# Optimization experiments

Measured on AMD Instinct MI355X. Metric: run time of the kernel, lower is better.

## Reference

```python
import jax, jax.numpy as jnp
import numpy as np

B, T, D, H = 2, 2048, 1024, 16
DH = D // H  # head dim = 64


def setup_inputs() -> dict:
    key = jax.random.key(0)
    ks = jax.random.split(key, 10)
    s = D ** -0.5
    inp = {
        "x": jax.random.normal(ks[0], (B, T, D), jnp.float32),
        "data_mask": jax.random.randint(ks[1], (B, T), 0, 2, jnp.int32),
        "Wq": jax.random.normal(ks[2], (D, D), jnp.float32) * s,
        "bq": jnp.zeros((D,), jnp.float32),
        "Wk": jax.random.normal(ks[3], (D, D), jnp.float32) * s,
        "bk": jnp.zeros((D,), jnp.float32),
        "Wv": jax.random.normal(ks[4], (D, D), jnp.float32) * s,
        "bv": jnp.zeros((D,), jnp.float32),
        "Wp": jax.random.normal(ks[5], (D, D), jnp.float32) * s,
        "bp": jnp.zeros((D,), jnp.float32),
    }
    return inp


def _split_heads(t):
    # [B, T, D] -> [B, H, T, DH]
    return jnp.swapaxes(t.reshape(B, T, H, DH), 1, 2)


def reference(x, data_mask, Wq, bq, Wk, bk, Wv, bv, Wp, bp):
    q = _split_heads(x @ Wq + bq)
    k = _split_heads(x @ Wk + bk)  # kv = x (self-attention)
    v = _split_heads(x @ Wv + bv)

    # combined mask: causal tri AND data_mask outer product -> [B, 1, T, T]
    dm = data_mask.astype(bool)
    causal = jnp.tril(jnp.ones((T, T), bool))
    mask = causal[None, None] & (dm[:, None, :, None] & dm[:, None, None, :])

    q = q * (DH ** -0.5)  # scale_logits
    scores = jnp.einsum('bhqd,bhkd->bhqk', q, k)  # [B, H, T, T]
    scores = jnp.where(mask, scores, -jnp.inf)
    weights = jax.nn.softmax(scores, axis=-1)
    weights = jnp.nan_to_num(weights)  # fully-masked rows -> 0
    o = jnp.einsum('bhqk,bhkd->bhqd', weights, v)

    # recover shape: [B, H, T, DH] -> [B, T, D]
    o = jnp.swapaxes(o, 1, 2).reshape(B, T, D)
    o = o @ Wp + bp

    # linear mask: multiply output by data_mask [B, T, 1]
    o = o * data_mask.astype(o.dtype)[..., None]
    return o
```

## Files before the change

### kernel.cpp

```cpp
#include <hip/hip_runtime.h>
#include <hip/hip_bf16.h>
#include <cstdint>
#include <cstddef>

#define Bb 2
#define Tt 2048
#define Dd 1024
#define Hh 16
#define DHh 64

using short8 = __attribute__((ext_vector_type(8))) short;
using f32x4  = __attribute__((ext_vector_type(4))) float;
typedef unsigned short u16;

__device__ __forceinline__ u16 f2bf(float f) {
    unsigned int u = __float_as_uint(f);
    u += 0x7fffu + ((u >> 16) & 1u);
    return (u16)(u >> 16);
}

__device__ __forceinline__ unsigned int pk2bf(float a, float b) {
    union { __hip_bfloat162 h; unsigned int u; } c;
    c.h = __float22bfloat162_rn(float2{a, b});
    return c.u;
}

__device__ __forceinline__ void gload16(const void* g, void* l) {
    __builtin_amdgcn_global_load_lds((const __attribute__((address_space(1))) void*)g,
                                     (__attribute__((address_space(3))) void*)l, 16, 0, 0);
}

__device__ __forceinline__ void gemm_bt_core(const u16* __restrict__ A, const u16* __restrict__ BT,
                                             int K, int m0, int n0,
                                             u16* As, u16* Bs, f32x4 acc[4][4]) {
    const int tid = threadIdx.x;
    const int w = tid >> 6, lane = tid & 63;
    const int lr = lane & 15, lg = lane >> 4;
    const int wr = w >> 1, wc = w & 1;
    const int arow = lane >> 2;
    const int acol = (lane & 3) * 8;
    for (int kk = 0; kk < K; kk += 32) {
        __syncthreads();
#pragma unroll
        for (int j = 0; j < 2; ++j) {
            int r0 = w * 32 + j * 16;
            gload16(A  + (size_t)(m0 + r0 + arow) * K + kk + acol, (char*)As + r0 * 64);
            gload16(BT + (size_t)(n0 + r0 + arow) * K + kk + acol, (char*)Bs + r0 * 64);
        }
        __syncthreads();
        short8 af[4], bfv[4];
#pragma unroll
        for (int m = 0; m < 4; ++m)
            af[m] = *(const short8*)((const char*)As + ((wr * 64 + m * 16 + lr) * 64 + lg * 16));
#pragma unroll
        for (int n = 0; n < 4; ++n)
            bfv[n] = *(const short8*)((const char*)Bs + ((wc * 64 + n * 16 + lr) * 64 + lg * 16));
#pragma unroll
        for (int m = 0; m < 4; ++m)
#pragma unroll
            for (int n = 0; n < 4; ++n)
                acc[m][n] = __builtin_amdgcn_mfma_f32_16x16x32_bf16(af[m], bfv[n], acc[m][n], 0, 0, 0);
    }
}

__global__ __launch_bounds__(256) void convert_x_k(const float4* __restrict__ x4,
                                                   ushort4* __restrict__ xb4, int n4) {
    int i = blockIdx.x * 256 + threadIdx.x;
    if (i >= n4) return;
    float4 v = x4[i];
    ushort4 o;
    o.x = f2bf(v.x); o.y = f2bf(v.y); o.z = f2bf(v.z); o.w = f2bf(v.w);
    xb4[i] = o;
}

__global__ void transpose_w_k(const float* __restrict__ Wq, const float* __restrict__ Wk,
                              const float* __restrict__ Wv, const float* __restrict__ Wp,
                              u16* __restrict__ wt) {
    __shared__ float tile[32][33];
    const int z = blockIdx.z;
    const float* W = (z == 0) ? Wq : (z == 1) ? Wk : (z == 2) ? Wv : Wp;
    const int n0 = blockIdx.x * 32, k0 = blockIdx.y * 32;
    const int tx = threadIdx.x, ty = threadIdx.y;
#pragma unroll
    for (int j = 0; j < 4; ++j)
        tile[ty + j * 8][tx] = W[(size_t)(k0 + ty + j * 8) * Dd + n0 + tx];
    __syncthreads();
    u16* outp = wt + (size_t)z * Dd * Dd;
#pragma unroll
    for (int j = 0; j < 4; ++j)
        outp[(size_t)(n0 + ty + j * 8) * Dd + k0 + tx] = f2bf(tile[tx][ty + j * 8]);
}

__global__ __launch_bounds__(256) void qkv_gemm_k(const u16* __restrict__ xb, const u16* __restrict__ wt,
        const float* __restrict__ bq, const float* __restrict__ bk, const float* __restrict__ bv,
        u16* __restrict__ Qg, u16* __restrict__ Kg, u16* __restrict__ VTg) {
    __shared__ alignas(16) u16 As[128 * 32];
    __shared__ alignas(16) u16 Bs[128 * 32];
    f32x4 acc[4][4];
    const f32x4 vzero = {0.f, 0.f, 0.f, 0.f};
#pragma unroll
    for (int m = 0; m < 4; ++m)
#pragma unroll
        for (int n = 0; n < 4; ++n) acc[m][n] = vzero;
    const int m0 = blockIdx.y * 128, n0 = blockIdx.x * 128;
    gemm_bt_core(xb, wt, 1024, m0, n0, As, Bs, acc);
    const int tid = threadIdx.x, w = tid >> 6, lane = tid & 63, lr = lane & 15, lg = lane >> 4;
    const int wr = w >> 1, wc = w & 1;
    const int sec = n0 >> 10;
    const float* bias = (sec == 0) ? bq : (sec == 1) ? bk : bv;
    u16* dst = (sec == 0) ? Qg : (sec == 1) ? Kg : VTg;
    const float qscale = (sec == 0) ? 0.125f * 1.4426950408889634f : 1.0f;
#pragma unroll
    for (int n = 0; n < 4; ++n) {
        int gn = n0 + wc * 64 + n * 16 + lr;
        int j = gn & 1023;
        float bj = bias[j];
        int h = j >> 6, dh = j & 63;
#pragma unroll
        for (int m = 0; m < 4; ++m) {
            int gmb = m0 + wr * 64 + m * 16 + 4 * lg;
#pragma unroll
            for (int i = 0; i < 4; ++i) {
                int gm = gmb + i;
                int b = gm >> 11, t = gm & 2047;
                float v = (acc[m][n][i] + bj) * qscale;
                size_t off;
                if (sec < 2) off = (((size_t)(b * Hh + h)) * Tt + t) * DHh + dh;
                else         off = (((size_t)(b * Hh + h)) * DHh + dh) * Tt + t;
                dst[off] = f2bf(v);
            }
        }
    }
}

__global__ __launch_bounds__(256) void attn_k(const u16* __restrict__ Qg, const u16* __restrict__ Kg,
        const u16* __restrict__ VTg, const int* __restrict__ dmask, u16* __restrict__ Og) {
    __shared__ alignas(16) u16 Ks[128 * 64];
    __shared__ alignas(16) u16 Vs[64 * 128];
    __shared__ alignas(16) u16 Ps[4][16 * 128];
    const int bh = blockIdx.x;
    const int qb = (int)gridDim.y - 1 - (int)blockIdx.y;
    const int b = bh >> 4, h = bh & 15;
    const int tid = threadIdx.x, w = tid >> 6, lane = tid & 63;
    const int lr = lane & 15, lg = lane >> 4;
    const int q0 = qb * 64 + w * 16;
    const int qrow = q0 + lr;
    const u16* Qbase = Qg + ((size_t)bh * Tt + q0) * DHh;
    short8 qf0 = *(const short8*)(Qbase + lr * DHh + lg * 8);
    short8 qf1 = *(const short8*)(Qbase + lr * DHh + 32 + lg * 8);
    const f32x4 vzero = {0.f, 0.f, 0.f, 0.f};
    float mrow = -1e30f, lrow = 0.f;
    f32x4 o[4];
#pragma unroll
    for (int n = 0; n < 4; ++n) o[n] = vzero;
    const int ktiles = (qb * 64 + 63) / 128 + 1;
    char* KsB = (char*)Ks; char* VsB = (char*)Vs; char* PsB = (char*)&Ps[w][0];

    for (int kt = 0; kt < ktiles; ++kt) {
        const int kbase = kt * 128;
        __syncthreads();
#pragma unroll
        for (int j = 0; j < 4; ++j) {
            int r0 = w * 32 + j * 8;
            int r = r0 + (lane >> 3);
            int cs = (lane & 7) ^ (r & 7);
            gload16(Kg + ((size_t)bh * Tt + kbase + r) * DHh + cs * 8, KsB + r0 * 128);
        }
#pragma unroll
        for (int j = 0; j < 4; ++j) {
            int r0 = w * 16 + j * 4;
            int r = r0 + (lane >> 4);
            int cs = (lane & 15) ^ (r & 7);
            gload16(VTg + ((size_t)bh * DHh + r) * Tt + kbase + cs * 8, VsB + r0 * 256);
        }
        __syncthreads();
        f32x4 s[8];
#pragma unroll
        for (int nf = 0; nf < 8; ++nf) {
            int r = nf * 16 + lr;
            short8 k0v = *(const short8*)(KsB + r * 128 + (((0 + lg) ^ (r & 7)) << 4));
            short8 k1v = *(const short8*)(KsB + r * 128 + (((4 + lg) ^ (r & 7)) << 4));
            f32x4 t0 = __builtin_amdgcn_mfma_f32_16x16x32_bf16(k0v, qf0, vzero, 0, 0, 0);
            s[nf] = __builtin_amdgcn_mfma_f32_16x16x32_bf16(k1v, qf1, t0, 0, 0, 0);
        }
        float4 km[8];
        {
            const int4* dmv = (const int4*)(dmask + (size_t)b * Tt + kbase);
#pragma unroll
            for (int nf = 0; nf < 8; ++nf) {
                int4 mi = dmv[4 * nf + lg];
                km[nf] = make_float4((float)mi.x, (float)mi.y, (float)mi.z, (float)mi.w);
            }
        }
        if (kbase + 127 > q0) {
#pragma unroll
            for (int nf = 0; nf < 8; ++nf) {
                int tk = kbase + 16 * nf + 4 * lg;
                if (tk + 0 > qrow) km[nf].x = 0.f;
                if (tk + 1 > qrow) km[nf].y = 0.f;
                if (tk + 2 > qrow) km[nf].z = 0.f;
                if (tk + 3 > qrow) km[nf].w = 0.f;
            }
        }
        float rm;
        {
            f32x4 m4 = s[0];
#pragma unroll
            for (int nf = 1; nf < 8; ++nf) {
                m4[0] = fmaxf(m4[0], s[nf][0]); m4[1] = fmaxf(m4[1], s[nf][1]);
                m4[2] = fmaxf(m4[2], s[nf][2]); m4[3] = fmaxf(m4[3], s[nf][3]);
            }
            rm = fmaxf(fmaxf(m4[0], m4[1]), fmaxf(m4[2], m4[3]));
            rm = fmaxf(rm, __shfl_xor(rm, 16));
            rm = fmaxf(rm, __shfl_xor(rm, 32));
        }
        float mn = fmaxf(mrow, rm);
        float sc = exp2f(mrow - mn);
        mrow = mn;
        lrow *= sc;
#pragma unroll
        for (int n = 0; n < 4; ++n) {
            o[n][0] *= sc; o[n][1] *= sc; o[n][2] *= sc; o[n][3] *= sc;
        }
        float rs = 0.f;
#pragma unroll
        for (int nf = 0; nf < 8; ++nf) {
            float p0 = exp2f(s[nf][0] - mn) * km[nf].x;
            float p1 = exp2f(s[nf][1] - mn) * km[nf].y;
            float p2 = exp2f(s[nf][2] - mn) * km[nf].z;
            float p3 = exp2f(s[nf][3] - mn) * km[nf].w;
            rs += (p0 + p1) + (p2 + p3);
            uint2 pw;
            pw.x = pk2bf(p0, p1);
            pw.y = pk2bf(p2, p3);
            *(uint2*)(PsB + lr * 256 + ((((2 * nf + (lg >> 1)) ^ (lr & 7))) << 4) + ((lg & 1) << 3)) = pw;
        }
        rs += __shfl_xor(rs, 16);
        rs += __shfl_xor(rs, 32);
        lrow += rs;
#pragma unroll
        for (int ks = 0; ks < 4; ++ks) {
            short8 pf = *(const short8*)(PsB + lr * 256 + ((((ks * 4 + lg)) ^ (lr & 7)) << 4));
#pragma unroll
            for (int n = 0; n < 4; ++n) {
                int rv = n * 16 + lr;
                short8 vf = *(const short8*)(VsB + rv * 256 + ((((ks * 4 + lg)) ^ (rv & 7)) << 4));
                o[n] = __builtin_amdgcn_mfma_f32_16x16x32_bf16(vf, pf, o[n], 0, 0, 0);
            }
        }
    }
    float inv = lrow > 0.f ? 1.0f / lrow : 0.f;
#pragma unroll
    for (int n = 0; n < 4; ++n) {
        uint2 pw;
        pw.x = pk2bf(o[n][0] * inv, o[n][1] * inv);
        pw.y = pk2bf(o[n][2] * inv, o[n][3] * inv);
        *(uint2*)(Og + ((size_t)(b * Tt + qrow)) * Dd + h * DHh + n * 16 + 4 * lg) = pw;
    }
}

__global__ __launch_bounds__(256) void out_gemm_k(const u16* __restrict__ Og, const u16* __restrict__ wpt,
        const float* __restrict__ bp, const int* __restrict__ dmask, float* __restrict__ out) {
    __shared__ alignas(16) u16 As[128 * 32];
    __shared__ alignas(16) u16 Bs[128 * 32];
    f32x4 acc[4][4];
    const f32x4 vzero = {0.f, 0.f, 0.f, 0.f};
#pragma unroll
    for (int m = 0; m < 4; ++m)
#pragma unroll
        for (int n = 0; n < 4; ++n) acc[m][n] = vzero;
    const int m0 = blockIdx.y * 128, n0 = blockIdx.x * 128;
    gemm_bt_core(Og, wpt, 1024, m0, n0, As, Bs, acc);
    const int tid = threadIdx.x, w = tid >> 6, lane = tid & 63, lr = lane & 15, lg = lane >> 4;
    const int wr = w >> 1, wc = w & 1;
#pragma unroll
    for (int n = 0; n < 4; ++n) {
        int gn = n0 + wc * 64 + n * 16 + lr;
        float bj = bp[gn];
#pragma unroll
        for (int m = 0; m < 4; ++m) {
            int gmb = m0 + wr * 64 + m * 16 + 4 * lg;
#pragma unroll
            for (int i = 0; i < 4; ++i) {
                int gm = gmb + i;
                float dmv = (float)dmask[gm];
                out[(size_t)gm * Dd + gn] = (acc[m][n][i] + bj) * dmv;
            }
        }
    }
}

extern "C" void kernel_launch(void* const* d_in, const int* in_sizes, int n_in,
                              void* d_out, int out_size, void* d_ws, size_t ws_size,
                              hipStream_t stream) {
    const float* x   = (const float*)d_in[0];
    const int*  dmask = (const int*)d_in[1];
    const float* Wq = (const float*)d_in[2];
    const float* bq = (const float*)d_in[3];
    const float* Wk = (const float*)d_in[4];
    const float* bk = (const float*)d_in[5];
    const float* Wv = (const float*)d_in[6];
    const float* bv = (const float*)d_in[7];
    const float* Wp = (const float*)d_in[8];
    const float* bp = (const float*)d_in[9];
    float* out = (float*)d_out;
    char* ws = (char*)d_ws;
    u16* xb  = (u16*)(ws);
    u16* wt  = (u16*)(ws + ((size_t)8 << 20));
    u16* Qg  = (u16*)(ws + ((size_t)16 << 20));
    u16* Kg  = (u16*)(ws + ((size_t)24 << 20));
    u16* VTg = (u16*)(ws + ((size_t)32 << 20));
    u16* Og  = xb;

    convert_x_k<<<dim3(4096), dim3(256), 0, stream>>>((const float4*)x, (ushort4*)xb, (Bb * Tt * Dd) / 4);
    transpose_w_k<<<dim3(32, 32, 4), dim3(32, 8), 0, stream>>>(Wq, Wk, Wv, Wp, wt);
    qkv_gemm_k<<<dim3(24, 32), dim3(256), 0, stream>>>(xb, wt, bq, bk, bv, Qg, Kg, VTg);
    attn_k<<<dim3(32, 32), dim3(256), 0, stream>>>(Qg, Kg, VTg, dmask, Og);
    out_gemm_k<<<dim3(8, 32), dim3(256), 0, stream>>>(Og, wt + (size_t)3 * Dd * Dd, bp, dmask, out);
}
```

Measured before the change: 132.3 us.

## Restructure attention with 32x32 MFMA, 128-row query blocks and double-buffered K/V tiles

Rewrites the attention kernel so each block handles 128 query rows (32 per wave) using 32x32x16 bf16 MFMAs. K/V tiles shrink to 64 keys and are double-buffered, so the next tile's async load overlaps compute. P is passed between lanes with cross-lane shuffles instead of an LDS round trip. The grid halves to 512 blocks, which lowers parallelism and makes per-block work more unbalanced across the causal range, and register pressure rises with the 16-wide accumulators.

```diff
diff --git a/kernel.cpp b/kernel.cpp
--- a/kernel.cpp
+++ b/kernel.cpp
@@ -11,6 +11,7 @@
 
 using short8 = __attribute__((ext_vector_type(8))) short;
 using f32x4  = __attribute__((ext_vector_type(4))) float;
+using f32x16 = __attribute__((ext_vector_type(16))) float;
 typedef unsigned short u16;
 
 __device__ __forceinline__ u16 f2bf(float f) {
@@ -133,129 +134,149 @@
     }
 }
 
-__global__ __launch_bounds__(256) void attn_k(const u16* __restrict__ Qg, const u16* __restrict__ Kg,
+__global__ __launch_bounds__(256, 2) void attn_k(const u16* __restrict__ Qg, const u16* __restrict__ Kg,
         const u16* __restrict__ VTg, const int* __restrict__ dmask, u16* __restrict__ Og) {
-    __shared__ alignas(16) u16 Ks[128 * 64];
-    __shared__ alignas(16) u16 Vs[64 * 128];
-    __shared__ alignas(16) u16 Ps[4][16 * 128];
+    __shared__ alignas(16) u16 Ks[2][64 * 64];
+    __shared__ alignas(16) u16 Vs[2][64 * 64];
     const int bh = blockIdx.x;
-    const int qb = (int)gridDim.y - 1 - (int)blockIdx.y;
+    const int qb = 15 - (int)blockIdx.y;
     const int b = bh >> 4, h = bh & 15;
     const int tid = threadIdx.x, w = tid >> 6, lane = tid & 63;
-    const int lr = lane & 15, lg = lane >> 4;
-    const int q0 = qb * 64 + w * 16;
-    const int qrow = q0 + lr;
-    const u16* Qbase = Qg + ((size_t)bh * Tt + q0) * DHh;
-    short8 qf0 = *(const short8*)(Qbase + lr * DHh + lg * 8);
-    short8 qf1 = *(const short8*)(Qbase + lr * DHh + 32 + lg * 8);
-    const f32x4 vzero = {0.f, 0.f, 0.f, 0.f};
+    const int lq = lane & 31, hi = lane >> 5;
+    const int q0w = qb * 128 + w * 32;
+    const int qrow = q0w + lq;
+    short8 qf[4];
+    {
+        const u16* Qbase = Qg + ((size_t)bh * Tt + qrow) * DHh;
+#pragma unroll
+        for (int ks = 0; ks < 4; ++ks) qf[ks] = *(const short8*)(Qbase + ks * 16 + hi * 8);
+    }
+    f32x16 ot0, ot1;
+#pragma unroll
+    for (int i = 0; i < 16; ++i) { ot0[i] = 0.f; ot1[i] = 0.f; }
     float mrow = -1e30f, lrow = 0.f;
-    f32x4 o[4];
-#pragma unroll
-    for (int n = 0; n < 4; ++n) o[n] = vzero;
-    const int ktiles = (qb * 64 + 63) / 128 + 1;
-    char* KsB = (char*)Ks; char* VsB = (char*)Vs; char* PsB = (char*)&Ps[w][0];
-
-    for (int kt = 0; kt < ktiles; ++kt) {
-        const int kbase = kt * 128;
+    const int rr = lane >> 3, cc = lane & 7;
+
+#define STAGE(BUF, KB) do { \
+    _Pragma("unroll") \
+    for (int j = 0; j < 2; ++j) { \
+        int r0 = w * 16 + j * 8; \
+        gload16(Kg  + ((size_t)bh * Tt  + (KB) + r0 + rr) * DHh + ((cc ^ rr) * 8), (char*)&Ks[BUF][0] + r0 * 128); \
+        gload16(VTg + ((size_t)bh * DHh + r0 + rr) * Tt + (KB) + ((cc ^ rr) * 8), (char*)&Vs[BUF][0] + r0 * 128); \
+    } } while (0)
+
+    const int nkt = 2 * qb + 2;
+    int buf = 0;
+    STAGE(0, 0);
+    __syncthreads();
+    for (int kt = 0; kt < nkt; ++kt) {
+        const int kb = kt * 64;
+        if (kt + 1 < nkt) {
+            if (buf) STAGE(0, kb + 64); else STAGE(1, kb + 64);
+        }
+        if (kb <= q0w + 31) {
+            const char* KsB = (const char*)&Ks[buf][0];
+            const char* VsB = (const char*)&Vs[buf][0];
+            const int swz = lq & 7;
+            f32x16 st0, st1;
+#pragma unroll
+            for (int i = 0; i < 16; ++i) { st0[i] = 0.f; st1[i] = 0.f; }
+#pragma unroll
+            for (int ks = 0; ks < 4; ++ks) {
+                short8 kf0 = *(const short8*)(KsB + lq * 128        + (((2 * ks + hi) ^ swz) << 4));
+                short8 kf1 = *(const short8*)(KsB + (32 + lq) * 128 + (((2 * ks + hi) ^ swz) << 4));
+                st0 = __builtin_amdgcn_mfma_f32_32x32x16_bf16(kf0, qf[ks], st0, 0, 0, 0);
+                st1 = __builtin_amdgcn_mfma_f32_32x32x16_bf16(kf1, qf[ks], st1, 0, 0, 0);
+            }
+            float4 km[8];
+            {
+                const int4* dmv = (const int4*)(dmask + (size_t)b * Tt + kb);
+#pragma unroll
+                for (int t = 0; t < 2; ++t)
+#pragma unroll
+                    for (int g = 0; g < 4; ++g) {
+                        int4 mi = dmv[t * 8 + g * 2 + hi];
+                        km[t * 4 + g] = make_float4((float)mi.x, (float)mi.y, (float)mi.z, (float)mi.w);
+                    }
+            }
+            if (kb + 63 > q0w) {
+#pragma unroll
+                for (int t = 0; t < 2; ++t)
+#pragma unroll
+                    for (int g = 0; g < 4; ++g) {
+                        int k4 = kb + 32 * t + 8 * g + 4 * hi;
+                        float4& m4 = km[t * 4 + g];
+                        if (k4 + 0 > qrow) m4.x = 0.f;
+                        if (k4 + 1 > qrow) m4.y = 0.f;
+                        if (k4 + 2 > qrow) m4.z = 0.f;
+                        if (k4 + 3 > qrow) m4.w = 0.f;
+                    }
+            }
+            float rm = st0[0];
+#pragma unroll
+            for (int i = 1; i < 16; ++i) rm = fmaxf(rm, st0[i]);
+#pragma unroll
+            for (int i = 0; i < 16; ++i) rm = fmaxf(rm, st1[i]);
+            rm = fmaxf(rm, __shfl_xor(rm, 32));
+            float mn = fmaxf(mrow, rm);
+            float sc = exp2f(mrow - mn);
+            mrow = mn;
+            lrow *= sc;
+#pragma unroll
+            for (int i = 0; i < 16; ++i) { ot0[i] *= sc; ot1[i] *= sc; }
+            float rs = 0.f;
+#pragma unroll
+            for (int s = 0; s < 4; ++s) {
+                float p[8];
+#pragma unroll
+                for (int e = 0; e < 8; ++e) {
+                    float sv = (s < 2) ? ((s & 1) ? st0[8 + e] : st0[e])
+                                       : ((s & 1) ? st1[8 + e] : st1[e]);
+                    float mv;
+                    {
+                        const float4& m4 = km[(s >> 1) * 4 + (s & 1) * 2 + (e >> 2)];
+                        int e3 = e & 3;
+                        mv = (e3 == 0) ? m4.x : (e3 == 1) ? m4.y : (e3 == 2) ? m4.z : m4.w;
+                    }
+                    p[e] = exp2f(sv - mn) * mv;
+                    rs += p[e];
+                }
+                unsigned a0 = pk2bf(p[0], p[1]), a1 = pk2bf(p[2], p[3]);
+                unsigned b0 = pk2bf(p[4], p[5]), b1 = pk2bf(p[6], p[7]);
+                unsigned sa0 = __shfl_xor(a0, 32), sa1 = __shfl_xor(a1, 32);
+                unsigned sb0 = __shfl_xor(b0, 32), sb1 = __shfl_xor(b1, 32);
+                union { uint4 u; short8 sv; } pf;
+                pf.u.x = hi ? sb0 : a0;
+                pf.u.y = hi ? sb1 : a1;
+                pf.u.z = hi ? b0 : sa0;
+                pf.u.w = hi ? b1 : sa1;
+                short8 vf0 = *(const short8*)(VsB + lq * 128        + (((2 * s + hi) ^ swz) << 4));
+                short8 vf1 = *(const short8*)(VsB + (32 + lq) * 128 + (((2 * s + hi) ^ swz) << 4));
+                ot0 = __builtin_amdgcn_mfma_f32_32x32x16_bf16(vf0, pf.sv, ot0, 0, 0, 0);
+                ot1 = __builtin_amdgcn_mfma_f32_32x32x16_bf16(vf1, pf.sv, ot1, 0, 0, 0);
+            }
+            rs += __shfl_xor(rs, 32);
+            lrow += rs;
+        }
         __syncthreads();
-#pragma unroll
-        for (int j = 0; j < 4; ++j) {
-            int r0 = w * 32 + j * 8;
-            int r = r0 + (lane >> 3);
-            int cs = (lane & 7) ^ (r & 7);
-            gload16(Kg + ((size_t)bh * Tt + kbase + r) * DHh + cs * 8, KsB + r0 * 128);
-        }
-#pragma unroll
-        for (int j = 0; j < 4; ++j) {
-            int r0 = w * 16 + j * 4;
-            int r = r0 + (lane >> 4);
-            int cs = (lane & 15) ^ (r & 7);
-            gload16(VTg + ((size_t)bh * DHh + r) * Tt + kbase + cs * 8, VsB + r0 * 256);
-        }
-        __syncthreads();
-        f32x4 s[8];
-#pragma unroll
-        for (int nf = 0; nf < 8; ++nf) {
-            int r = nf * 16 + lr;
-            short8 k0v = *(const short8*)(KsB + r * 128 + (((0 + lg) ^ (r & 7)) << 4));
-            short8 k1v = *(const short8*)(KsB + r * 128 + (((4 + lg) ^ (r & 7)) << 4));
-            f32x4 t0 = __builtin_amdgcn_mfma_f32_16x16x32_bf16(k0v, qf0, vzero, 0, 0, 0);
-            s[nf] = __builtin_amdgcn_mfma_f32_16x16x32_bf16(k1v, qf1, t0, 0, 0, 0);
-        }
-        float4 km[8];
-        {
-            const int4* dmv = (const int4*)(dmask + (size_t)b * Tt + kbase);
-#pragma unroll
-            for (int nf = 0; nf < 8; ++nf) {
-                int4 mi = dmv[4 * nf + lg];
-                km[nf] = make_float4((float)mi.x, (float)mi.y, (float)mi.z, (float)mi.w);
-            }
-        }
-        if (kbase + 127 > q0) {
-#pragma unroll
-            for (int nf = 0; nf < 8; ++nf) {
-                int tk = kbase + 16 * nf + 4 * lg;
-                if (tk + 0 > qrow) km[nf].x = 0.f;
-                if (tk + 1 > qrow) km[nf].y = 0.f;
-                if (tk + 2 > qrow) km[nf].z = 0.f;
-                if (tk + 3 > qrow) km[nf].w = 0.f;
-            }
-        }
-        float rm;
-        {
-            f32x4 m4 = s[0];
-#pragma unroll
-            for (int nf = 1; nf < 8; ++nf) {
-                m4[0] = fmaxf(m4[0], s[nf][0]); m4[1] = fmaxf(m4[1], s[nf][1]);
-                m4[2] = fmaxf(m4[2], s[nf][2]); m4[3] = fmaxf(m4[3], s[nf][3]);
-            }
-            rm = fmaxf(fmaxf(m4[0], m4[1]), fmaxf(m4[2], m4[3]));
-            rm = fmaxf(rm, __shfl_xor(rm, 16));
-            rm = fmaxf(rm, __shfl_xor(rm, 32));
-        }
-        float mn = fmaxf(mrow, rm);
-        float sc = exp2f(mrow - mn);
-        mrow = mn;
-        lrow *= sc;
-#pragma unroll
-        for (int n = 0; n < 4; ++n) {
-            o[n][0] *= sc; o[n][1] *= sc; o[n][2] *= sc; o[n][3] *= sc;
-        }
-        float rs = 0.f;
-#pragma unroll
-        for (int nf = 0; nf < 8; ++nf) {
-            float p0 = exp2f(s[nf][0] - mn) * km[nf].x;
-            float p1 = exp2f(s[nf][1] - mn) * km[nf].y;
-            float p2 = exp2f(s[nf][2] - mn) * km[nf].z;
-            float p3 = exp2f(s[nf][3] - mn) * km[nf].w;
-            rs += (p0 + p1) + (p2 + p3);
+        buf ^= 1;
+    }
+#undef STAGE
+    float inv = lrow > 0.f ? 1.0f / lrow : 0.f;
+    u16* ob = Og + ((size_t)(b * Tt + qrow)) * Dd + h * DHh;
+#pragma unroll
+    for (int d = 0; d < 2; ++d) {
+#pragma unroll
+        for (int g = 0; g < 4; ++g) {
             uint2 pw;
-            pw.x = pk2bf(p0, p1);
-            pw.y = pk2bf(p2, p3);
-            *(uint2*)(PsB + lr * 256 + ((((2 * nf + (lg >> 1)) ^ (lr & 7))) << 4) + ((lg & 1) << 3)) = pw;
-        }
-        rs += __shfl_xor(rs, 16);
-        rs += __shfl_xor(rs, 32);
-        lrow += rs;
-#pragma unroll
-        for (int ks = 0; ks < 4; ++ks) {
-            short8 pf = *(const short8*)(PsB + lr * 256 + ((((ks * 4 + lg)) ^ (lr & 7)) << 4));
-#pragma unroll
-            for (int n = 0; n < 4; ++n) {
-                int rv = n * 16 + lr;
-                short8 vf = *(const short8*)(VsB + rv * 256 + ((((ks * 4 + lg)) ^ (rv & 7)) << 4));
-                o[n] = __builtin_amdgcn_mfma_f32_16x16x32_bf16(vf, pf, o[n], 0, 0, 0);
-            }
-        }
-    }
-    float inv = lrow > 0.f ? 1.0f / lrow : 0.f;
-#pragma unroll
-    for (int n = 0; n < 4; ++n) {
-        uint2 pw;
-        pw.x = pk2bf(o[n][0] * inv, o[n][1] * inv);
-        pw.y = pk2bf(o[n][2] * inv, o[n][3] * inv);
-        *(uint2*)(Og + ((size_t)(b * Tt + qrow)) * Dd + h * DHh + n * 16 + 4 * lg) = pw;
+            float v0 = (d ? ot1[4 * g + 0] : ot0[4 * g + 0]) * inv;
+            float v1 = (d ? ot1[4 * g + 1] : ot0[4 * g + 1]) * inv;
+            float v2 = (d ? ot1[4 * g + 2] : ot0[4 * g + 2]) * inv;
+            float v3 = (d ? ot1[4 * g + 3] : ot0[4 * g + 3]) * inv;
+            pw.x = pk2bf(v0, v1);
+            pw.y = pk2bf(v2, v3);
+            *(uint2*)(ob + d * 32 + g * 8 + hi * 4) = pw;
+        }
     }
 }
 
@@ -315,6 +336,6 @@
     convert_x_k<<<dim3(4096), dim3(256), 0, stream>>>((const float4*)x, (ushort4*)xb, (Bb * Tt * Dd) / 4);
     transpose_w_k<<<dim3(32, 32, 4), dim3(32, 8), 0, stream>>>(Wq, Wk, Wv, Wp, wt);
     qkv_gemm_k<<<dim3(24, 32), dim3(256), 0, stream>>>(xb, wt, bq, bk, bv, Qg, Kg, VTg);
-    attn_k<<<dim3(32, 32), dim3(256), 0, stream>>>(Qg, Kg, VTg, dmask, Og);
+    attn_k<<<dim3(32, 16), dim3(256), 0, stream>>>(Qg, Kg, VTg, dmask, Og);
     out_gemm_k<<<dim3(8, 32), dim3(256), 0, stream>>>(Og, wt + (size_t)3 * Dd * Dd, bp, dmask, out);
 }
```

Result: slower. 147.8 us (+11.7%).

## Replace QKV GEMM with 256x256-tile, 8-wave double-buffered pipelined kernel

Applied to the files above, without the earlier changes.

Rewrites the QKV projection GEMM as a 512-thread kernel with 256x256 output tiles, K-step 64 and double-buffered LDS. Quarter-tile global staging is interleaved with MFMA phases under explicit barriers and waitcnt, and MFMA runs at raised priority. A block-index swizzle is added for L2 locality, along with XOR-swizzled LDS layout. The aim is to hide global-load latency and raise MFMA utilization. The cost is heavy register and LDS use (128KB LDS), only 192 blocks on the device, and fragile hand-written synchronization.

```diff
diff --git a/kernel.cpp b/kernel.cpp
--- a/kernel.cpp
+++ b/kernel.cpp
@@ -91,34 +91,119 @@
         outp[(size_t)(n0 + ty + j * 8) * Dd + k0 + tx] = f2bf(tile[tx][ty + j * 8]);
 }
 
-__global__ __launch_bounds__(256) void qkv_gemm_k(const u16* __restrict__ xb, const u16* __restrict__ wt,
+#define BARX() do { asm volatile("" ::: "memory"); __builtin_amdgcn_s_barrier(); asm volatile("" ::: "memory"); } while (0)
+#define LGKM0() asm volatile("s_waitcnt lgkmcnt(0)" ::: "memory")
+#define VMC2()  asm volatile("s_waitcnt vmcnt(2)" ::: "memory")
+
+__global__ __launch_bounds__(512, 2) void qkv_gemm8_k(const u16* __restrict__ xb, const u16* __restrict__ wt,
         const float* __restrict__ bq, const float* __restrict__ bk, const float* __restrict__ bv,
         u16* __restrict__ Qg, u16* __restrict__ Kg, u16* __restrict__ VTg) {
-    __shared__ alignas(16) u16 As[128 * 32];
-    __shared__ alignas(16) u16 Bs[128 * 32];
-    f32x4 acc[4][4];
-    const f32x4 vzero = {0.f, 0.f, 0.f, 0.f};
-#pragma unroll
-    for (int m = 0; m < 4; ++m)
-#pragma unroll
-        for (int n = 0; n < 4; ++n) acc[m][n] = vzero;
-    const int m0 = blockIdx.y * 128, n0 = blockIdx.x * 128;
-    gemm_bt_core(xb, wt, 1024, m0, n0, As, Bs, acc);
-    const int tid = threadIdx.x, w = tid >> 6, lane = tid & 63, lr = lane & 15, lg = lane >> 4;
-    const int wr = w >> 1, wc = w & 1;
-    const int sec = n0 >> 10;
+    __shared__ alignas(16) u16 lds[2][4][128 * 64];
+    const int tid = threadIdx.x;
+    const int wid = tid >> 6, lane = tid & 63;
+    const int lr = lane & 15, lg = lane >> 4;
+    const int wm = wid >> 2, wn = wid & 3;
+    const int wuni = wid;
+    const int bid = (int)blockIdx.x;
+    const int swzb = (bid & 7) * 24 + (bid >> 3);
+    const int bx = swzb % 12, by = swzb / 12;
+    const int bm0 = by * 256, bn0 = bx * 256;
+    const u16* hsrc[4] = { xb + (size_t)bm0 * 1024,
+                           xb + (size_t)(bm0 + 128) * 1024,
+                           wt + (size_t)bn0 * 1024,
+                           wt + (size_t)(bn0 + 128) * 1024 };
+    const int swzr = ((lr >> 2) & 1) << 1;
+
+#define STAGE_H(BUF, H, TI) do { \
+    const u16* sb_ = hsrc[H]; \
+    const int kk_ = (((TI) < 15) ? (TI) : 15) * 64; \
+    _Pragma("unroll") \
+    for (int j_ = 0; j_ < 2; ++j_) { \
+        int tj_ = tid + j_ * 512; \
+        int row_ = tj_ >> 3; \
+        int cs_ = (tj_ & 7) ^ (((tj_ >> 5) & 1) << 1); \
+        gload16(sb_ + (size_t)row_ * 1024 + kk_ + cs_ * 8, \
+                (char*)&lds[BUF][H][0] + wuni * 1024 + j_ * 8192); \
+    } } while (0)
+
+    short8 af[2][4], bf[2][2];
+#define DSREAD_A(BUF, MQ) do { \
+    _Pragma("unroll") \
+    for (int ks_ = 0; ks_ < 2; ++ks_) \
+    _Pragma("unroll") \
+    for (int mm_ = 0; mm_ < 4; ++mm_) { \
+        int ra_ = (MQ) * 64 + mm_ * 16 + lr; \
+        af[ks_][mm_] = *(const short8*)((const char*)&lds[BUF][wm][0] + ra_ * 128 + (((ks_ * 4 + lg) ^ swzr) << 4)); \
+    } } while (0)
+#define DSREAD_B(BUF, NQ) do { \
+    _Pragma("unroll") \
+    for (int ks_ = 0; ks_ < 2; ++ks_) \
+    _Pragma("unroll") \
+    for (int nn_ = 0; nn_ < 2; ++nn_) { \
+        int rb_ = (wn & 1) * 64 + (NQ) * 32 + nn_ * 16 + lr; \
+        bf[ks_][nn_] = *(const short8*)((const char*)&lds[BUF][2 + (wn >> 1)][0] + rb_ * 128 + (((ks_ * 4 + lg) ^ swzr) << 4)); \
+    } } while (0)
+
+    f32x4 acc[8][4];
+#pragma unroll
+    for (int m = 0; m < 8; ++m)
+#pragma unroll
+        for (int n = 0; n < 4; ++n) acc[m][n] = f32x4{0.f, 0.f, 0.f, 0.f};
+
+#define MFMAQ(MQ, NQ) do { \
+    __builtin_amdgcn_s_setprio(1); \
+    _Pragma("unroll") \
+    for (int mm_ = 0; mm_ < 4; ++mm_) \
+    _Pragma("unroll") \
+    for (int nn_ = 0; nn_ < 2; ++nn_) \
+    _Pragma("unroll") \
+    for (int ks_ = 0; ks_ < 2; ++ks_) \
+        acc[(MQ) * 4 + mm_][(NQ) * 2 + nn_] = __builtin_amdgcn_mfma_f32_16x16x32_bf16(af[ks_][mm_], bf[ks_][nn_], acc[(MQ) * 4 + mm_][(NQ) * 2 + nn_], 0, 0, 0); \
+    __builtin_amdgcn_s_setprio(0); \
+    } while (0)
+
+    STAGE_H(0, 0, 0); STAGE_H(0, 1, 0); STAGE_H(0, 2, 0); STAGE_H(0, 3, 0);
+    STAGE_H(1, 0, 1);
+    VMC2();
+    BARX();
+
+    for (int i = 0; i < 8; ++i) {
+        const int t1 = 2 * i + 1, t2 = 2 * i + 2, t3 = 2 * i + 3;
+        DSREAD_A(0, 0); DSREAD_B(0, 0); STAGE_H(1, 1, t1);
+        BARX(); LGKM0(); MFMAQ(0, 0); BARX();
+        DSREAD_B(0, 1); STAGE_H(1, 2, t1);
+        BARX(); LGKM0(); MFMAQ(0, 1); BARX();
+        DSREAD_A(0, 1); STAGE_H(1, 3, t1);
+        BARX(); LGKM0(); MFMAQ(1, 1); BARX();
+        DSREAD_B(0, 0); STAGE_H(0, 0, t2); VMC2();
+        BARX(); LGKM0(); MFMAQ(1, 0); BARX();
+        DSREAD_A(1, 0); DSREAD_B(1, 0); STAGE_H(0, 1, t2);
+        BARX(); LGKM0(); MFMAQ(0, 0); BARX();
+        DSREAD_B(1, 1); STAGE_H(0, 2, t2);
+        BARX(); LGKM0(); MFMAQ(0, 1); BARX();
+        DSREAD_A(1, 1); STAGE_H(0, 3, t2);
+        BARX(); LGKM0(); MFMAQ(1, 1); BARX();
+        DSREAD_B(1, 0); STAGE_H(1, 0, t3); VMC2();
+        BARX(); LGKM0(); MFMAQ(1, 0); BARX();
+    }
+#undef STAGE_H
+#undef DSREAD_A
+#undef DSREAD_B
+#undef MFMAQ
+
+    const int sec = bn0 >> 10;
     const float* bias = (sec == 0) ? bq : (sec == 1) ? bk : bv;
     u16* dst = (sec == 0) ? Qg : (sec == 1) ? Kg : VTg;
     const float qscale = (sec == 0) ? 0.125f * 1.4426950408889634f : 1.0f;
 #pragma unroll
     for (int n = 0; n < 4; ++n) {
-        int gn = n0 + wc * 64 + n * 16 + lr;
+        int gn = bn0 + wn * 64 + n * 16 + lr;
         int j = gn & 1023;
         float bj = bias[j];
         int h = j >> 6, dh = j & 63;
 #pragma unroll
-        for (int m = 0; m < 4; ++m) {
-            int gmb = m0 + wr * 64 + m * 16 + 4 * lg;
+        for (int m = 0; m < 8; ++m) {
+            int gmb = bm0 + wm * 128 + m * 16 + 4 * lg;
 #pragma unroll
             for (int i = 0; i < 4; ++i) {
                 int gm = gmb + i;
@@ -314,7 +399,7 @@
 
     convert_x_k<<<dim3(4096), dim3(256), 0, stream>>>((const float4*)x, (ushort4*)xb, (Bb * Tt * Dd) / 4);
     transpose_w_k<<<dim3(32, 32, 4), dim3(32, 8), 0, stream>>>(Wq, Wk, Wv, Wp, wt);
-    qkv_gemm_k<<<dim3(24, 32), dim3(256), 0, stream>>>(xb, wt, bq, bk, bv, Qg, Kg, VTg);
+    qkv_gemm8_k<<<dim3(192), dim3(512), 0, stream>>>(xb, wt, bq, bk, bv, Qg, Kg, VTg);
     attn_k<<<dim3(32, 32), dim3(256), 0, stream>>>(Qg, Kg, VTg, dmask, Og);
     out_gemm_k<<<dim3(8, 32), dim3(256), 0, stream>>>(Og, wt + (size_t)3 * Dd * Dd, bp, dmask, out);
 }
```

Result: slower. 153.1 us (+15.7%).
